# Optimization experiments

Hardware: AMD Instinct MI355X
Metric: run time of the kernel (lower is better)

## Reference

```python
import jax, jax.numpy as jnp
import numpy as np
import math

# dims
C2, C1, T = 32, 64, 2048      # x shape
AVGF = 32                     # num_submatrices
SEG = T // AVGF               # 64
M = C1 * C2                   # M_size1 = 2048
TK = 3                        # num_blocks
HA = 16                       # num_heads
DH = M // HA                  # 128
EPS = 1e-5


def setup_inputs() -> dict:
    key = jax.random.key(0)
    ks = jax.random.split(key, 12)
    sc = 0.02  # scale params to keep fp32 activations finite
    return {
        "x": jax.random.normal(ks[0], (C2, C1, T), dtype=jnp.float32),
        "weight": jax.random.normal(ks[1], (M, M), dtype=jnp.float32) * sc,
        "Wqkv": jax.random.normal(ks[2], (TK, 3, HA, DH, M), dtype=jnp.float32) * sc,
        "Wo": jax.random.normal(ks[3], (TK, M, M), dtype=jnp.float32) * sc,
        "ln1_g": jnp.ones((M,), jnp.float32),
        "ln1_b": jnp.zeros((M,), jnp.float32),
        "ln2_g": jnp.ones((M,), jnp.float32),
        "ln2_b": jnp.zeros((M,), jnp.float32),
        "fc1_w": jax.random.normal(ks[4], (4 * M, M), dtype=jnp.float32) * sc,
        "fc1_b": jnp.zeros((4 * M,), jnp.float32),
        "fc2_w": jax.random.normal(ks[5], (M, 4 * M), dtype=jnp.float32) * sc,
        "fc2_b": jnp.zeros((M,), jnp.float32),
    }


def _ln(x, g, b):
    mu = jnp.mean(x, axis=-1, keepdims=True)
    var = jnp.var(x, axis=-1, keepdims=True)
    return (x - mu) / jnp.sqrt(var + EPS) * g + b


def _sinusoidal_bias():
    # bias[i, 2j]   = sin(i / 10000**(2*(2j)/M))  -- exponent uses even column index
    # bias[i, 2j+1] = cos(same angle)
    i = jnp.arange(AVGF, dtype=jnp.float32)[:, None]          # [avgf, 1]
    j = jnp.arange(0, M, 2, dtype=jnp.float32)[None, :]       # [1, M/2] even cols
    ang = i / jnp.power(10000.0, 2.0 * j / M)                 # [avgf, M/2]
    return jnp.stack([jnp.sin(ang), jnp.cos(ang)], axis=-1).reshape(AVGF, M)


def reference(x, weight, Wqkv, Wo, ln1_g, ln1_b, ln2_g, ln2_b,
              fc1_w, fc1_b, fc2_w, fc2_b):
    inp = jnp.transpose(x, (2, 1, 0))                          # [T, C1, C2]
    # segment-average over time -> [avgf, C1, C2]
    inputc = inp.reshape(AVGF, SEG, C1, C2).mean(axis=1)
    altx = inputc.reshape(AVGF, M)                             # [avgf, M]
    s = jnp.einsum('lm,im->il', weight, altx)                  # [avgf, M]
    s = s + _sinusoidal_bias()
    inv_sqrt_dh = 1.0 / math.sqrt(DH)
    for a in range(TK):                                        # fixed small block loop
        y = _ln(s, ln1_g, ln1_b)
        qkv = jnp.einsum('xhdm,im->xihd', Wqkv[a], y)          # [3, avgf, hA, Dh]
        q, k, v = qkv[0], qkv[1], qkv[2]
        rsa = jnp.einsum('ihd,ihd->ih', q * inv_sqrt_dh, k)    # per-token scalar attn
        imv = jnp.cumsum(rsa[..., None] * v, axis=0)           # serial inter-block scan
        s = jnp.einsum('nm,im->in', Wo[a], imv.reshape(AVGF, M)) + s
        s = _ln(s, ln2_g, ln2_b) + s
        h = jax.nn.gelu(s @ fc1_w.T + fc1_b, approximate=False)
        s = h @ fc2_w.T + fc2_b
    return s.reshape(AVGF, C1, C2)
```

## Files before the change

kernel.cpp:

```cpp
#include <hip/hip_runtime.h>
#include <math.h>

typedef __attribute__((ext_vector_type(4))) float f32x4;
typedef __attribute__((ext_vector_type(8))) short bf16x8;

__device__ inline short f2bf(float f) {
    union { float f; unsigned u; } v; v.f = f;
    unsigned u = v.u;
    u += 0x7fffu + ((u >> 16) & 1u);
    return (short)(u >> 16);
}

__global__ __launch_bounds__(256) void k_avg_init(const float* __restrict__ x,
                                                  float* __restrict__ altx,
                                                  float* __restrict__ s) {
    int blk = blockIdx.x, t = threadIdx.x;
    if (blk < 512) {
        int wv = t >> 6, lane = t & 63;
        int p = blk * 4 + wv;
        const float* row = x + (size_t)p * 2048;
        int c2 = p >> 6, c1 = p & 63;
        int m = c1 * 32 + c2;
        for (int seg = 0; seg < 32; ++seg) {
            float v = row[seg * 64 + lane];
            for (int off = 32; off; off >>= 1) v += __shfl_xor(v, off, 64);
            if (lane == 0) altx[seg * 2048 + m] = v * (1.0f / 64.0f);
        }
    } else {
        int i = blk - 512;
        const float kln = logf(10000.0f) / 1024.0f;
        for (int l = t; l < 2048; l += 256) {
            int c = l & ~1;
            float ang = (float)i * expf(-(float)c * kln);
            s[i * 2048 + l] = (l & 1) ? cosf(ang) : sinf(ang);
        }
    }
}

__device__ inline void row_stats(const float* __restrict__ row, float& mu, float& rstd) {
    float sm = 0.f, ss = 0.f;
    for (int idx = threadIdx.x; idx < 2048; idx += 256) {
        float v = row[idx]; sm += v; ss += v * v;
    }
    for (int off = 32; off; off >>= 1) {
        sm += __shfl_xor(sm, off, 64);
        ss += __shfl_xor(ss, off, 64);
    }
    __shared__ float as[4], bs[4];
    int wv = threadIdx.x >> 6, lane = threadIdx.x & 63;
    if (lane == 0) { as[wv] = sm; bs[wv] = ss; }
    __syncthreads();
    sm = as[0] + as[1] + as[2] + as[3];
    ss = bs[0] + bs[1] + bs[2] + bs[3];
    mu = sm * (1.0f / 2048.0f);
    float var = ss * (1.0f / 2048.0f) - mu * mu;
    rstd = rsqrtf(var + 1e-5f);
}

__global__ __launch_bounds__(256) void k_prep1(const float* __restrict__ s,
                                               const float* __restrict__ g,
                                               const float* __restrict__ b,
                                               float* __restrict__ y,
                                               float* __restrict__ qkv) {
    int blk = blockIdx.x;
    if (blk < 32) {
        const float* row = s + blk * 2048;
        float mu, rstd; row_stats(row, mu, rstd);
        float* yr = y + blk * 2048;
        for (int idx = threadIdx.x; idx < 2048; idx += 256)
            yr[idx] = (row[idx] - mu) * rstd * g[idx] + b[idx];
    } else {
        int z = blk - 32;
        float4* p4 = (float4*)(qkv + (size_t)z * 8192);
        float4 zero = {0.f, 0.f, 0.f, 0.f};
        for (int idx = threadIdx.x; idx < 2048; idx += 256) p4[idx] = zero;
    }
}

__global__ __launch_bounds__(256) void k_scan(const float* __restrict__ qkv,
                                              const float* __restrict__ s,
                                              float* __restrict__ imv,
                                              float* __restrict__ s2) {
    int blk = blockIdx.x, t = threadIdx.x;
    if (blk < 16) {
        int h = blk;
        __shared__ float rsa[32];
        if (t < 32) {
            const float* qr = qkv + (size_t)t * 6144 + h * 128;
            const float* kr = qr + 2048;
            float acc = 0.f;
            for (int d = 0; d < 128; ++d) acc += qr[d] * kr[d];
            rsa[t] = acc * 0.08838834764831845f;
        }
        __syncthreads();
        if (t < 128) {
            float acc = 0.f;
            for (int i = 0; i < 32; ++i) {
                acc += rsa[i] * qkv[(size_t)i * 6144 + 4096 + h * 128 + t];
                imv[i * 2048 + h * 128 + t] = acc;
            }
        }
    } else {
        int z = blk - 16;
        const float4* sp = (const float4*)(s + (size_t)z * 2048);
        float4* dp = (float4*)(s2 + (size_t)z * 2048);
        for (int idx = t; idx < 512; idx += 256) dp[idx] = sp[idx];
    }
}

__global__ __launch_bounds__(256) void k_prep2(const float* __restrict__ s2,
                                               const float* __restrict__ g,
                                               const float* __restrict__ b,
                                               float* __restrict__ sout,
                                               float* __restrict__ h) {
    int blk = blockIdx.x;
    if (blk < 32) {
        const float* row = s2 + blk * 2048;
        float mu, rstd; row_stats(row, mu, rstd);
        float* sr = sout + blk * 2048;
        for (int idx = threadIdx.x; idx < 2048; idx += 256) {
            float v = row[idx];
            sr[idx] = (v - mu) * rstd * g[idx] + b[idx] + v;
        }
    } else {
        int z = blk - 32;
        float4* p4 = (float4*)(h + (size_t)z * 8192);
        float4 zero = {0.f, 0.f, 0.f, 0.f};
        for (int idx = threadIdx.x; idx < 2048; idx += 256) p4[idx] = zero;
    }
}

__global__ __launch_bounds__(256) void k_act(float* __restrict__ h,
                                             const float* __restrict__ fc1_b,
                                             float* __restrict__ sout,
                                             const float* __restrict__ fc2_b) {
    int blk = blockIdx.x, t = threadIdx.x;
    if (blk < 128) {
        size_t base = ((size_t)blk * 256 + t) * 8;
        #pragma unroll
        for (int j = 0; j < 8; ++j) {
            size_t idx = base + j;
            float v = h[idx] + fc1_b[idx & 8191];
            h[idx] = 0.5f * v * (1.0f + erff(v * 0.70710678118654752f));
        }
    } else {
        size_t base = ((size_t)(blk - 128) * 256 + t) * 8;
        #pragma unroll
        for (int j = 0; j < 8; ++j) {
            size_t idx = base + j;
            sout[idx] = fc2_b[idx & 2047];
        }
    }
}

template<int NIT>
__global__ __launch_bounds__(256, 2) void k_gemm(const float* __restrict__ W,
                                                 const float* __restrict__ act,
                                                 float* __restrict__ out,
                                                 int N, int K) {
    int t = threadIdx.x;
    int lane = t & 63, wv = t >> 6;
    int m = lane & 15, q = lane >> 4;
    int nb = blockIdx.x * 64 + wv * 16;
    size_t kbeg = (size_t)blockIdx.y * (NIT * 32);
    const float* A0 = act + (size_t)m * K + kbeg + q * 8;
    const float* A1 = A0 + (size_t)16 * K;
    const float* B  = W + (size_t)(nb + m) * K + kbeg + q * 8;
    f32x4 acc0 = {0.f, 0.f, 0.f, 0.f};
    f32x4 acc1 = {0.f, 0.f, 0.f, 0.f};

    float4 a0l = *(const float4*)(A0);
    float4 a0h = *(const float4*)(A0 + 4);
    float4 a1l = *(const float4*)(A1);
    float4 a1h = *(const float4*)(A1 + 4);
    float4 bl  = *(const float4*)(B);
    float4 bh  = *(const float4*)(B + 4);

    #pragma unroll
    for (int it = 0; it < NIT; ++it) {
        float4 c0l = a0l, c0h = a0h, c1l = a1l, c1h = a1h, cbl = bl, cbh = bh;
        if (it + 1 < NIT) {
            int k = (it + 1) * 32;
            a0l = *(const float4*)(A0 + k);
            a0h = *(const float4*)(A0 + k + 4);
            a1l = *(const float4*)(A1 + k);
            a1h = *(const float4*)(A1 + k + 4);
            bl  = *(const float4*)(B + k);
            bh  = *(const float4*)(B + k + 4);
        }
        bf16x8 fa0 = { f2bf(c0l.x), f2bf(c0l.y), f2bf(c0l.z), f2bf(c0l.w),
                       f2bf(c0h.x), f2bf(c0h.y), f2bf(c0h.z), f2bf(c0h.w) };
        bf16x8 fa1 = { f2bf(c1l.x), f2bf(c1l.y), f2bf(c1l.z), f2bf(c1l.w),
                       f2bf(c1h.x), f2bf(c1h.y), f2bf(c1h.z), f2bf(c1h.w) };
        bf16x8 fb  = { f2bf(cbl.x), f2bf(cbl.y), f2bf(cbl.z), f2bf(cbl.w),
                       f2bf(cbh.x), f2bf(cbh.y), f2bf(cbh.z), f2bf(cbh.w) };
        acc0 = __builtin_amdgcn_mfma_f32_16x16x32_bf16(fa0, fb, acc0, 0, 0, 0);
        acc1 = __builtin_amdgcn_mfma_f32_16x16x32_bf16(fa1, fb, acc1, 0, 0, 0);
    }
    float* op = out + (size_t)(q * 4) * N + nb + m;
    #pragma unroll
    for (int r = 0; r < 4; ++r) {
        atomicAdd(op + (size_t)r * N, acc0[r]);
        atomicAdd(op + (size_t)(r + 16) * N, acc1[r]);
    }
}

extern "C" void kernel_launch(void* const* d_in, const int* in_sizes, int n_in,
                              void* d_out, int out_size, void* d_ws, size_t ws_size,
                              hipStream_t stream) {
    const float* x      = (const float*)d_in[0];
    const float* weight = (const float*)d_in[1];
    const float* Wqkv   = (const float*)d_in[2];
    const float* Wo     = (const float*)d_in[3];
    const float* ln1_g  = (const float*)d_in[4];
    const float* ln1_b  = (const float*)d_in[5];
    const float* ln2_g  = (const float*)d_in[6];
    const float* ln2_b  = (const float*)d_in[7];
    const float* fc1_w  = (const float*)d_in[8];
    const float* fc1_b  = (const float*)d_in[9];
    const float* fc2_w  = (const float*)d_in[10];
    const float* fc2_b  = (const float*)d_in[11];
    float* ws   = (float*)d_ws;
    float* altx = ws;
    float* sbuf = ws + 65536;
    float* y    = ws + 131072;
    float* s2   = ws + 196608;
    float* imv  = ws + 262144;
    float* qkv  = ws + 327680;
    float* h    = ws + 524288;
    float* outF = (float*)d_out;

    k_avg_init<<<544, 256, 0, stream>>>(x, altx, sbuf);
    k_gemm<4><<<dim3(32, 16), 256, 0, stream>>>(weight, altx, sbuf, 2048, 2048);
    for (int a = 0; a < 3; ++a) {
        k_prep1<<<56, 256, 0, stream>>>(sbuf, ln1_g, ln1_b, y, qkv);
        k_gemm<4><<<dim3(96, 16), 256, 0, stream>>>(Wqkv + (size_t)a * 12582912, y, qkv, 6144, 2048);
        k_scan<<<48, 256, 0, stream>>>(qkv, sbuf, imv, s2);
        k_gemm<4><<<dim3(32, 16), 256, 0, stream>>>(Wo + (size_t)a * 4194304, imv, s2, 2048, 2048);
        k_prep2<<<64, 256, 0, stream>>>(s2, ln2_g, ln2_b, sbuf, h);
        k_gemm<4><<<dim3(128, 16), 256, 0, stream>>>(fc1_w, sbuf, h, 8192, 2048);
        float* sout = (a == 2) ? outF : sbuf;
        k_act<<<160, 256, 0, stream>>>(h, fc1_b, sout, fc2_b);
        k_gemm<4><<<dim3(32, 64), 256, 0, stream>>>(fc2_w, h, sout, 2048, 8192);
    }
}
```

Baseline: 618.8 us.

## Fuse elementwise stages into GEMM tails via completion counters and spin-wait

```diff
diff --git a/kernel.cpp b/kernel.cpp
--- a/kernel.cpp
+++ b/kernel.cpp
@@ -11,10 +11,29 @@
     return (short)(u >> 16);
 }
 
-__global__ __launch_bounds__(256) void k_avg_init(const float* __restrict__ x,
-                                                  float* __restrict__ altx,
-                                                  float* __restrict__ s) {
+#define WS_ALTX 0
+#define WS_SBUF 65536
+#define WS_Y    131072
+#define WS_IMV  196608
+#define WS_QKV  262144
+#define WS_H    458752
+#define WS_CNT  720896
+
+struct P {
+    const float* W; const float* A; float* out;
+    int N, K, NX, NS;
+    int* cnt;
+    const float* g1; const float* b1; const float* g2; const float* b2;
+    const float* fc1_b; const float* fc2_b;
+    float* sbuf; float* y; float* qkv; float* imv; float* h; float* outF;
+    int a;
+    float* zbuf; int z4;
+};
+
+__global__ __launch_bounds__(256) void k_init(const float* __restrict__ x, float* __restrict__ ws) {
     int blk = blockIdx.x, t = threadIdx.x;
+    float* altx = ws + WS_ALTX;
+    float* sbuf = ws + WS_SBUF;
     if (blk < 512) {
         int wv = t >> 6, lane = t & 63;
         int p = blk * 4 + wv;
@@ -26,67 +45,155 @@
             for (int off = 32; off; off >>= 1) v += __shfl_xor(v, off, 64);
             if (lane == 0) altx[seg * 2048 + m] = v * (1.0f / 64.0f);
         }
-    } else {
+    } else if (blk < 544) {
         int i = blk - 512;
         const float kln = logf(10000.0f) / 1024.0f;
         for (int l = t; l < 2048; l += 256) {
             int c = l & ~1;
             float ang = (float)i * expf(-(float)c * kln);
-            s[i * 2048 + l] = (l & 1) ? cosf(ang) : sinf(ang);
-        }
-    }
-}
-
-__device__ inline void row_stats(const float* __restrict__ row, float& mu, float& rstd) {
-    float sm = 0.f, ss = 0.f;
-    for (int idx = threadIdx.x; idx < 2048; idx += 256) {
-        float v = row[idx]; sm += v; ss += v * v;
-    }
+            sbuf[i * 2048 + l] = (l & 1) ? cosf(ang) : sinf(ang);
+        }
+    } else if (blk == 544) {
+        if (t < 16) ((int*)(ws + WS_CNT))[t] = 0;
+    } else if (blk < 569) {
+        float4* zp = (float4*)(ws + WS_QKV);
+        float4 z = {0.f,0.f,0.f,0.f};
+        int base = (blk - 545) * 2048;
+        #pragma unroll
+        for (int j = 0; j < 8; ++j) zp[base + t + j * 256] = z;
+    } else {
+        float4* zp = (float4*)(ws + WS_H);
+        float4 z = {0.f,0.f,0.f,0.f};
+        int base = (blk - 569) * 2048;
+        #pragma unroll
+        for (int j = 0; j < 8; ++j) zp[base + t + j * 256] = z;
+    }
+}
+
+__device__ inline void red2(float& sm, float& ss) {
     for (int off = 32; off; off >>= 1) {
         sm += __shfl_xor(sm, off, 64);
         ss += __shfl_xor(ss, off, 64);
     }
-    __shared__ float as[4], bs[4];
+    __shared__ float ra[4], rb[4];
     int wv = threadIdx.x >> 6, lane = threadIdx.x & 63;
-    if (lane == 0) { as[wv] = sm; bs[wv] = ss; }
+    if (lane == 0) { ra[wv] = sm; rb[wv] = ss; }
     __syncthreads();
-    sm = as[0] + as[1] + as[2] + as[3];
-    ss = bs[0] + bs[1] + bs[2] + bs[3];
-    mu = sm * (1.0f / 2048.0f);
-    float var = ss * (1.0f / 2048.0f) - mu * mu;
-    rstd = rsqrtf(var + 1e-5f);
-}
-
-__global__ __launch_bounds__(256) void k_prep1(const float* __restrict__ s,
-                                               const float* __restrict__ g,
-                                               const float* __restrict__ b,
-                                               float* __restrict__ y,
-                                               float* __restrict__ qkv) {
-    int blk = blockIdx.x;
-    if (blk < 32) {
-        const float* row = s + blk * 2048;
-        float mu, rstd; row_stats(row, mu, rstd);
-        float* yr = y + blk * 2048;
-        for (int idx = threadIdx.x; idx < 2048; idx += 256)
-            yr[idx] = (row[idx] - mu) * rstd * g[idx] + b[idx];
-    } else {
-        int z = blk - 32;
-        float4* p4 = (float4*)(qkv + (size_t)z * 8192);
-        float4 zero = {0.f, 0.f, 0.f, 0.f};
-        for (int idx = threadIdx.x; idx < 2048; idx += 256) p4[idx] = zero;
-    }
-}
-
-__global__ __launch_bounds__(256) void k_scan(const float* __restrict__ qkv,
-                                              const float* __restrict__ s,
-                                              float* __restrict__ imv,
-                                              float* __restrict__ s2) {
-    int blk = blockIdx.x, t = threadIdx.x;
-    if (blk < 16) {
-        int h = blk;
+    sm = ra[0] + ra[1] + ra[2] + ra[3];
+    ss = rb[0] + rb[1] + rb[2] + rb[3];
+}
+
+template<int NIT, int TAIL>
+__global__ __launch_bounds__(256, 2) void k_gemm(P p) {
+    int t = threadIdx.x;
+
+    if ((int)blockIdx.y >= p.NS) {
+        int per = (p.z4 + p.NX - 1) / p.NX;
+        float4* zp = (float4*)p.zbuf;
+        float4 z = {0.f,0.f,0.f,0.f};
+        int base = blockIdx.x * per, end = min(base + per, p.z4);
+        for (int i = base + t; i < end; i += 256) zp[i] = z;
+        return;
+    }
+
+    {
+        int lane = t & 63, wv = t >> 6;
+        int m = lane & 15, q = lane >> 4;
+        int nb = blockIdx.x * 64 + wv * 16;
+        int K = p.K, N = p.N;
+        size_t kbeg = (size_t)blockIdx.y * (NIT * 32);
+        const float* A0 = p.A + (size_t)m * K + kbeg + q * 8;
+        const float* A1 = A0 + (size_t)16 * K;
+        const float* B  = p.W + (size_t)(nb + m) * K + kbeg + q * 8;
+        f32x4 acc0 = {0.f,0.f,0.f,0.f};
+        f32x4 acc1 = {0.f,0.f,0.f,0.f};
+        float4 a0l = *(const float4*)(A0);
+        float4 a0h = *(const float4*)(A0 + 4);
+        float4 a1l = *(const float4*)(A1);
+        float4 a1h = *(const float4*)(A1 + 4);
+        float4 bl  = *(const float4*)(B);
+        float4 bh  = *(const float4*)(B + 4);
+        #pragma unroll
+        for (int it = 0; it < NIT; ++it) {
+            float4 c0l = a0l, c0h = a0h, c1l = a1l, c1h = a1h, cbl = bl, cbh = bh;
+            if (it + 1 < NIT) {
+                int k = (it + 1) * 32;
+                a0l = *(const float4*)(A0 + k);
+                a0h = *(const float4*)(A0 + k + 4);
+                a1l = *(const float4*)(A1 + k);
+                a1h = *(const float4*)(A1 + k + 4);
+                bl  = *(const float4*)(B + k);
+                bh  = *(const float4*)(B + k + 4);
+            }
+            bf16x8 fa0 = { f2bf(c0l.x), f2bf(c0l.y), f2bf(c0l.z), f2bf(c0l.w),
+                           f2bf(c0h.x), f2bf(c0h.y), f2bf(c0h.z), f2bf(c0h.w) };
+            bf16x8 fa1 = { f2bf(c1l.x), f2bf(c1l.y), f2bf(c1l.z), f2bf(c1l.w),
+                           f2bf(c1h.x), f2bf(c1h.y), f2bf(c1h.z), f2bf(c1h.w) };
+            bf16x8 fb  = { f2bf(cbl.x), f2bf(cbl.y), f2bf(cbl.z), f2bf(cbl.w),
+                           f2bf(cbh.x), f2bf(cbh.y), f2bf(cbh.z), f2bf(cbh.w) };
+            acc0 = __builtin_amdgcn_mfma_f32_16x16x32_bf16(fa0, fb, acc0, 0, 0, 0);
+            acc1 = __builtin_amdgcn_mfma_f32_16x16x32_bf16(fa1, fb, acc1, 0, 0, 0);
+        }
+        float* op = p.out + (size_t)(q * 4) * N + nb + m;
+        #pragma unroll
+        for (int r = 0; r < 4; ++r) {
+            atomicAdd(op + (size_t)r * N, acc0[r]);
+            atomicAdd(op + (size_t)(r + 16) * N, acc1[r]);
+        }
+    }
+
+    __syncthreads();
+    if (t == 0) {
+        __threadfence();
+        __hip_atomic_fetch_add(p.cnt, 1, __ATOMIC_RELEASE, __HIP_MEMORY_SCOPE_AGENT);
+    }
+    if (TAIL == 0) return;
+
+    constexpr int NTAIL = (TAIL == 2) ? 16 : (TAIL == 4) ? 64 : 32;
+    if (blockIdx.y != 0 || (int)blockIdx.x >= NTAIL) return;
+
+    int target = p.NX * p.NS;
+    if (t == 0) {
+        while (__hip_atomic_load(p.cnt, __ATOMIC_ACQUIRE, __HIP_MEMORY_SCOPE_AGENT) < target)
+            __builtin_amdgcn_s_sleep(8);
+    }
+    __syncthreads();
+    __threadfence();
+
+    if (TAIL == 1 || TAIL == 3 || TAIL == 5) {
+        int r = blockIdx.x;
+        const float* row = p.sbuf + r * 2048;
+        float vv[8], sm = 0.f, ss = 0.f;
+        #pragma unroll
+        for (int j = 0; j < 8; ++j) {
+            int idx = t + j * 256;
+            float v = row[idx];
+            if (TAIL == 5) v += p.fc2_b[idx];
+            vv[j] = v; sm += v; ss += v * v;
+        }
+        red2(sm, ss);
+        float mu = sm * (1.0f / 2048.0f);
+        float rstd = rsqrtf(ss * (1.0f / 2048.0f) - mu * mu + 1e-5f);
+        if (TAIL == 5 && p.a == 2) {
+            #pragma unroll
+            for (int j = 0; j < 8; ++j) p.outF[r * 2048 + t + j * 256] = vv[j];
+        } else {
+            #pragma unroll
+            for (int j = 0; j < 8; ++j) {
+                int idx = t + j * 256;
+                float v = vv[j];
+                float ln1 = (v - mu) * rstd * p.g1[idx] + p.b1[idx];
+                if (TAIL == 1) p.y[r * 2048 + idx] = ln1;
+                if (TAIL == 3) p.sbuf[r * 2048 + idx] = (v - mu) * rstd * p.g2[idx] + p.b2[idx] + v;
+                if (TAIL == 5) { p.sbuf[r * 2048 + idx] = v; p.y[r * 2048 + idx] = ln1; }
+            }
+        }
+    }
+    if (TAIL == 2) {
+        int hd = blockIdx.x;
         __shared__ float rsa[32];
         if (t < 32) {
-            const float* qr = qkv + (size_t)t * 6144 + h * 128;
+            const float* qr = p.qkv + (size_t)t * 6144 + hd * 128;
             const float* kr = qr + 2048;
             float acc = 0.f;
             for (int d = 0; d < 128; ++d) acc += qr[d] * kr[d];
@@ -96,112 +203,23 @@
         if (t < 128) {
             float acc = 0.f;
             for (int i = 0; i < 32; ++i) {
-                acc += rsa[i] * qkv[(size_t)i * 6144 + 4096 + h * 128 + t];
-                imv[i * 2048 + h * 128 + t] = acc;
+                acc += rsa[i] * p.qkv[(size_t)i * 6144 + 4096 + hd * 128 + t];
+                p.imv[i * 2048 + hd * 128 + t] = acc;
             }
         }
-    } else {
-        int z = blk - 16;
-        const float4* sp = (const float4*)(s + (size_t)z * 2048);
-        float4* dp = (float4*)(s2 + (size_t)z * 2048);
-        for (int idx = t; idx < 512; idx += 256) dp[idx] = sp[idx];
-    }
-}
-
-__global__ __launch_bounds__(256) void k_prep2(const float* __restrict__ s2,
-                                               const float* __restrict__ g,
-                                               const float* __restrict__ b,
-                                               float* __restrict__ sout,
-                                               float* __restrict__ h) {
-    int blk = blockIdx.x;
-    if (blk < 32) {
-        const float* row = s2 + blk * 2048;
-        float mu, rstd; row_stats(row, mu, rstd);
-        float* sr = sout + blk * 2048;
-        for (int idx = threadIdx.x; idx < 2048; idx += 256) {
-            float v = row[idx];
-            sr[idx] = (v - mu) * rstd * g[idx] + b[idx] + v;
-        }
-    } else {
-        int z = blk - 32;
-        float4* p4 = (float4*)(h + (size_t)z * 8192);
-        float4 zero = {0.f, 0.f, 0.f, 0.f};
-        for (int idx = threadIdx.x; idx < 2048; idx += 256) p4[idx] = zero;
-    }
-}
-
-__global__ __launch_bounds__(256) void k_act(float* __restrict__ h,
-                                             const float* __restrict__ fc1_b,
-                                             float* __restrict__ sout,
-                                             const float* __restrict__ fc2_b) {
-    int blk = blockIdx.x, t = threadIdx.x;
-    if (blk < 128) {
-        size_t base = ((size_t)blk * 256 + t) * 8;
-        #pragma unroll
-        for (int j = 0; j < 8; ++j) {
-            size_t idx = base + j;
-            float v = h[idx] + fc1_b[idx & 8191];
-            h[idx] = 0.5f * v * (1.0f + erff(v * 0.70710678118654752f));
-        }
-    } else {
-        size_t base = ((size_t)(blk - 128) * 256 + t) * 8;
-        #pragma unroll
-        for (int j = 0; j < 8; ++j) {
-            size_t idx = base + j;
-            sout[idx] = fc2_b[idx & 2047];
-        }
-    }
-}
-
-template<int NIT>
-__global__ __launch_bounds__(256, 2) void k_gemm(const float* __restrict__ W,
-                                                 const float* __restrict__ act,
-                                                 float* __restrict__ out,
-                                                 int N, int K) {
-    int t = threadIdx.x;
-    int lane = t & 63, wv = t >> 6;
-    int m = lane & 15, q = lane >> 4;
-    int nb = blockIdx.x * 64 + wv * 16;
-    size_t kbeg = (size_t)blockIdx.y * (NIT * 32);
-    const float* A0 = act + (size_t)m * K + kbeg + q * 8;
-    const float* A1 = A0 + (size_t)16 * K;
-    const float* B  = W + (size_t)(nb + m) * K + kbeg + q * 8;
-    f32x4 acc0 = {0.f, 0.f, 0.f, 0.f};
-    f32x4 acc1 = {0.f, 0.f, 0.f, 0.f};
-
-    float4 a0l = *(const float4*)(A0);
-    float4 a0h = *(const float4*)(A0 + 4);
-    float4 a1l = *(const float4*)(A1);
-    float4 a1h = *(const float4*)(A1 + 4);
-    float4 bl  = *(const float4*)(B);
-    float4 bh  = *(const float4*)(B + 4);
-
-    #pragma unroll
-    for (int it = 0; it < NIT; ++it) {
-        float4 c0l = a0l, c0h = a0h, c1l = a1l, c1h = a1h, cbl = bl, cbh = bh;
-        if (it + 1 < NIT) {
-            int k = (it + 1) * 32;
-            a0l = *(const float4*)(A0 + k);
-            a0h = *(const float4*)(A0 + k + 4);
-            a1l = *(const float4*)(A1 + k);
-            a1h = *(const float4*)(A1 + k + 4);
-            bl  = *(const float4*)(B + k);
-            bh  = *(const float4*)(B + k + 4);
-        }
-        bf16x8 fa0 = { f2bf(c0l.x), f2bf(c0l.y), f2bf(c0l.z), f2bf(c0l.w),
-                       f2bf(c0h.x), f2bf(c0h.y), f2bf(c0h.z), f2bf(c0h.w) };
-        bf16x8 fa1 = { f2bf(c1l.x), f2bf(c1l.y), f2bf(c1l.z), f2bf(c1l.w),
-                       f2bf(c1h.x), f2bf(c1h.y), f2bf(c1h.z), f2bf(c1h.w) };
-        bf16x8 fb  = { f2bf(cbl.x), f2bf(cbl.y), f2bf(cbl.z), f2bf(cbl.w),
-                       f2bf(cbh.x), f2bf(cbh.y), f2bf(cbh.z), f2bf(cbh.w) };
-        acc0 = __builtin_amdgcn_mfma_f32_16x16x32_bf16(fa0, fb, acc0, 0, 0, 0);
-        acc1 = __builtin_amdgcn_mfma_f32_16x16x32_bf16(fa1, fb, acc1, 0, 0, 0);
-    }
-    float* op = out + (size_t)(q * 4) * N + nb + m;
-    #pragma unroll
-    for (int r = 0; r < 4; ++r) {
-        atomicAdd(op + (size_t)r * N, acc0[r]);
-        atomicAdd(op + (size_t)(r + 16) * N, acc1[r]);
+    }
+    if (TAIL == 4) {
+        int b = blockIdx.x;
+        size_t base = (size_t)b * 4096;
+        #pragma unroll
+        for (int j = 0; j < 16; ++j) {
+            size_t idx = base + t + j * 256;
+            float v = p.h[idx] + p.fc1_b[idx & 8191];
+            p.h[idx] = 0.5f * v * (1.0f + erff(v * 0.70710678118654752f));
+        }
+        float4* zp = (float4*)p.sbuf;
+        float4 z = {0.f,0.f,0.f,0.f};
+        zp[b * 256 + t] = z;
     }
 }
 
@@ -220,27 +238,43 @@
     const float* fc1_b  = (const float*)d_in[9];
     const float* fc2_w  = (const float*)d_in[10];
     const float* fc2_b  = (const float*)d_in[11];
-    float* ws   = (float*)d_ws;
-    float* altx = ws;
-    float* sbuf = ws + 65536;
-    float* y    = ws + 131072;
-    float* s2   = ws + 196608;
-    float* imv  = ws + 262144;
-    float* qkv  = ws + 327680;
-    float* h    = ws + 524288;
-    float* outF = (float*)d_out;
-
-    k_avg_init<<<544, 256, 0, stream>>>(x, altx, sbuf);
-    k_gemm<4><<<dim3(32, 16), 256, 0, stream>>>(weight, altx, sbuf, 2048, 2048);
+    float* ws = (float*)d_ws;
+    int* cnt = (int*)(ws + WS_CNT);
+
+    P base{};
+    base.g1 = ln1_g; base.b1 = ln1_b; base.g2 = ln2_g; base.b2 = ln2_b;
+    base.fc1_b = fc1_b; base.fc2_b = fc2_b;
+    base.sbuf = ws + WS_SBUF; base.y = ws + WS_Y; base.qkv = ws + WS_QKV;
+    base.imv = ws + WS_IMV; base.h = ws + WS_H; base.outF = (float*)d_out;
+
+    k_init<<<601, 256, 0, stream>>>(x, ws);
+
+    P p = base;
+    p.W = weight; p.A = ws + WS_ALTX; p.out = ws + WS_SBUF;
+    p.N = 2048; p.K = 2048; p.NX = 32; p.NS = 8; p.cnt = cnt + 0; p.z4 = 0;
+    k_gemm<8, 1><<<dim3(32, 8), 256, 0, stream>>>(p);
+
     for (int a = 0; a < 3; ++a) {
-        k_prep1<<<56, 256, 0, stream>>>(sbuf, ln1_g, ln1_b, y, qkv);
-        k_gemm<4><<<dim3(96, 16), 256, 0, stream>>>(Wqkv + (size_t)a * 12582912, y, qkv, 6144, 2048);
-        k_scan<<<48, 256, 0, stream>>>(qkv, sbuf, imv, s2);
-        k_gemm<4><<<dim3(32, 16), 256, 0, stream>>>(Wo + (size_t)a * 4194304, imv, s2, 2048, 2048);
-        k_prep2<<<64, 256, 0, stream>>>(s2, ln2_g, ln2_b, sbuf, h);
-        k_gemm<4><<<dim3(128, 16), 256, 0, stream>>>(fc1_w, sbuf, h, 8192, 2048);
-        float* sout = (a == 2) ? outF : sbuf;
-        k_act<<<160, 256, 0, stream>>>(h, fc1_b, sout, fc2_b);
-        k_gemm<4><<<dim3(32, 64), 256, 0, stream>>>(fc2_w, h, sout, 2048, 8192);
-    }
-}
+        P q = base; q.a = a;
+        q.W = Wqkv + (size_t)a * 12582912; q.A = ws + WS_Y; q.out = ws + WS_QKV;
+        q.N = 6144; q.K = 2048; q.NX = 96; q.NS = 8; q.cnt = cnt + 1 + a * 4;
+        q.zbuf = ws + WS_H; q.z4 = (a > 0) ? 65536 : 0;
+        k_gemm<8, 2><<<dim3(96, 8 + (q.z4 ? 1 : 0)), 256, 0, stream>>>(q);
+
+        P w = base; w.a = a;
+        w.W = Wo + (size_t)a * 4194304; w.A = ws + WS_IMV; w.out = ws + WS_SBUF;
+        w.N = 2048; w.K = 2048; w.NX = 32; w.NS = 8; w.cnt = cnt + 2 + a * 4; w.z4 = 0;
+        k_gemm<8, 3><<<dim3(32, 8), 256, 0, stream>>>(w);
+
+        P f1 = base; f1.a = a;
+        f1.W = fc1_w; f1.A = ws + WS_SBUF; f1.out = ws + WS_H;
+        f1.N = 8192; f1.K = 2048; f1.NX = 128; f1.NS = 8; f1.cnt = cnt + 3 + a * 4;
+        f1.zbuf = ws + WS_QKV; f1.z4 = (a < 2) ? 49152 : 0;
+        k_gemm<8, 4><<<dim3(128, 8 + (f1.z4 ? 1 : 0)), 256, 0, stream>>>(f1);
+
+        P f2 = base; f2.a = a;
+        f2.W = fc2_w; f2.A = ws + WS_H; f2.out = ws + WS_SBUF;
+        f2.N = 2048; f2.K = 8192; f2.NX = 32; f2.NS = 32; f2.cnt = cnt + 4 + a * 4; f2.z4 = 0;
+        k_gemm<8, 5><<<dim3(32, 32), 256, 0, stream>>>(f2);
+    }
+}
```

After: 1.197 ms. +93.5%, slower.
